# Performance work log

Measured on AMD Instinct MI355X. Metric: run time of the kernel, lower is better.

The kernel has to match this reference:

```python
import jax, jax.numpy as jnp
import numpy as np

F = 16       # num_field
D = 64       # embedding dim
N = 100000   # vocab size n
B = 2048     # batch
ORDER = 3
BETA = 1e-4
H = 64       # policy hidden (policy_layer=[64])


def build_levels(num_field, order):
    """Static reconstruction of create_mask recursion as integer index lists.
    At level t: V0 has r rows (row a = field a + t - 1); V_cur column k carries
    threshold thr[k]; the boolean mask is mask[a,k] = (a >= thr[k]); entries are
    enumerated row-major (matching torch boolean indexing). M_minus zeroes the
    last row (a == r-1) before the next level."""
    levels = []
    thr = np.arange(num_field - 1)  # create_mask(eye(F)) -> lower-tri incl diag
    r = num_field - 1
    for _ in range(2, order + 1):
        a_grid, k_grid = np.meshgrid(np.arange(r), np.arange(len(thr)), indexing='ij')
        sel = a_grid >= thr[None, :]
        rows = a_grid[sel]            # V0 row per selected interaction
        cols = k_grid[sel]            # V_cur column per selected interaction
        keep = np.nonzero(rows <= r - 2)[0]  # M_minus: drop last-row entries
        levels.append((rows, cols, keep))
        thr = rows[keep]
        r -= 1
    return levels

LEVELS = build_levels(F, ORDER)


def setup_inputs():
    key = jax.random.key(0)
    ks = jax.random.split(key, 9)
    x = jax.random.randint(ks[0], (B, F), 0, N)
    M = jax.random.normal(ks[1], (F, F), jnp.float32)
    w0 = jax.random.normal(ks[2], (1,), jnp.float32) * 0.01
    w_table = jax.random.normal(ks[3], (N,), jnp.float32) * 0.01
    V_table = jax.random.normal(ks[4], (N, D), jnp.float32) * 0.01
    Z_table = jax.random.normal(ks[5], (N, D), jnp.float32) * 0.01
    W1 = jax.random.normal(ks[6], (D, H), jnp.float32) * (1.0 / np.sqrt(D))
    b1 = jnp.zeros((H,), jnp.float32)
    W2 = jax.random.normal(ks[7], (H, 1), jnp.float32) * (1.0 / np.sqrt(H))
    b2 = jnp.zeros((1,), jnp.float32)
    return {"x": x, "M": M, "w0": w0, "w_table": w_table, "V_table": V_table,
            "Z_table": Z_table, "W1": W1, "b1": b1, "W2": W2, "b2": b2}


def reference(x, M, w0, w_table, V_table, Z_table, W1, b1, W2, b2):
    # forward_infer path (select=False)
    w = w_table[x]                                 # [B, F]
    V = V_table[x]                                 # [B, F, D]
    Z = jax.lax.stop_gradient(Z_table[x])          # .detach() in torch
    V0f = jnp.einsum('fg,bgd->bfd', M, V)          # M @ V
    Z0f = jnp.einsum('fg,bgd->bfd', M, Z)
    V_cur, V0 = V0f[:, :-1], V0f[:, 1:]
    Z_cur, Z0 = Z0f[:, :-1], Z0f[:, 1:]
    y = w0[0] + jnp.sum(w, axis=1)                 # [B]
    eps_key = jax.random.key(42)
    for li, (rows, cols, keep) in enumerate(LEVELS):
        # masked outer products, only at valid unique-combination slots
        V_sel = V0[:, rows] * V_cur[:, cols]       # [B, P, D]
        Z_sel = Z0[:, rows] * Z_cur[:, cols]       # [B, P, D]
        Wt = jnp.sum(V_sel, axis=-1)               # inference(): [B, P]
        h = jax.nn.relu(Z_sel @ W1 + b1)
        pro = jax.nn.sigmoid(h @ W2 + b2)[..., 0]  # [B, P]
        eps = jax.random.uniform(jax.random.fold_in(eps_key, li), pro.shape)
        S = (pro >= eps).astype(jnp.float32)       # Bernoulli selection
        y = y + jnp.sum(Wt * S, axis=-1)
        # slice for next order: V = V[:, M_minus]; V0 = V0[:, 1:]
        V_cur, Z_cur = V_sel[:, keep], Z_sel[:, keep]
        V0, Z0 = V0[:, 1:], Z0[:, 1:]
    regular = BETA * (jnp.sum(w * w) + jnp.sum(V_cur * V_cur))
    return y, regular
```

## Files before the change

kernel.cpp:

```cpp
#include <hip/hip_runtime.h>
#include <stdint.h>
#include <math.h>

#define NB    2048
#define NE    680
#define L1N   120
#define L2N   560
#define KEEP2 455
#define ROWP  68
#define NT    43
#define WLOS  72

#define THREEFRY_PARTITIONABLE 1

typedef __attribute__((ext_vector_type(8))) short bf16x8;
typedef __attribute__((ext_vector_type(4))) float f32x4;

union ABfrag { bf16x8 v; uint32_t u[4]; };

__device__ __forceinline__ uint32_t rotl32(uint32_t v, uint32_t d) {
  return (v << d) | (v >> (32u - d));
}

__device__ __forceinline__ uint32_t bf_rne(float f) {
  uint32_t u = __float_as_uint(f);
  return (u + 0x7fffu + ((u >> 16) & 1u)) >> 16;
}

__device__ __forceinline__ void tf2x32(uint32_t k0, uint32_t k1,
                                       uint32_t c0, uint32_t c1,
                                       uint32_t &o0, uint32_t &o1) {
  uint32_t ks2 = k0 ^ k1 ^ 0x1BD11BDAu;
  uint32_t x0 = c0 + k0;
  uint32_t x1 = c1 + k1;
#define TF_R(r) { x0 += x1; x1 = rotl32(x1, r); x1 ^= x0; }
  TF_R(13) TF_R(15) TF_R(26) TF_R(6)
  x0 += k1;  x1 += ks2 + 1u;
  TF_R(17) TF_R(29) TF_R(16) TF_R(24)
  x0 += ks2; x1 += k0 + 2u;
  TF_R(13) TF_R(15) TF_R(26) TF_R(6)
  x0 += k0;  x1 += k1 + 3u;
  TF_R(17) TF_R(29) TF_R(16) TF_R(24)
  x0 += k1;  x1 += ks2 + 4u;
  TF_R(13) TF_R(15) TF_R(26) TF_R(6)
  x0 += ks2; x1 += k0 + 5u;
#undef TF_R
  o0 = x0; o1 = x1;
}

__global__ __launch_bounds__(256, 8) void sfis_main(
    const int*   __restrict__ x,
    const float* __restrict__ M,
    const float* __restrict__ w0,
    const float* __restrict__ w_table,
    const float* __restrict__ V_table,
    const float* __restrict__ Z_table,
    const float* __restrict__ W1,
    const float* __restrict__ b1,
    const float* __restrict__ W2,
    const float* __restrict__ b2,
    float* __restrict__ out,
    float* __restrict__ reg_partial) {
  __shared__ __align__(16) float V0s[17 * ROWP];
  __shared__ __align__(16) float Z0s[17 * ROWP];
  __shared__ __align__(16) unsigned short W1loT[64 * WLOS];
  __shared__ unsigned short descs16[NT * 16];
  __shared__ float wts[NT * 16];
  __shared__ float t2s[NT * 16];
  __shared__ float W2s[64];
  __shared__ int xs[16];
  __shared__ float red8[8];
  __shared__ float wsum_s, w2sum_s;

  const int b   = blockIdx.x;
  const int tid = threadIdx.x;

  if (tid < 16) xs[tid] = x[b * 16 + tid];
  if (tid < 64) {
    W2s[tid] = W2[tid];
    V0s[16 * ROWP + tid] = 1.f;
    Z0s[16 * ROWP + tid] = 1.f;
  }
  for (int e = tid; e < NT * 16; e += 256) {
    int fi, fj, fl, lvl;
    if (e < L1N) {
      int a = 0;
      while ((a + 1) * (a + 2) / 2 <= e) ++a;
      int k = e - a * (a + 1) / 2;
      fi = a + 1; fj = k; fl = 16; lvl = 0;
    } else if (e < NE) {
      int e2 = e - L1N;
      int A = 0;
      while ((A + 1) * (A + 2) * (A + 3) / 6 <= e2) ++A;
      int k = e2 - A * (A + 1) * (A + 2) / 6;
      int a1 = 0;
      while ((a1 + 1) * (a1 + 2) / 2 <= k) ++a1;
      int k1 = k - a1 * (a1 + 1) / 2;
      fi = A + 2; fj = a1 + 1; fl = k1; lvl = 1;
    } else {
      fi = 16; fj = 16; fl = 16; lvl = 0;
    }
    descs16[e] = (unsigned short)((uint32_t)fi | ((uint32_t)fj << 5) |
                                  ((uint32_t)fl << 10) | ((uint32_t)lvl << 15));
  }
  for (int i = tid; i < 4096; i += 256) {
    int n = i & 63, k = i >> 6;
    float w = W1[i];
    uint32_t hb = bf_rne(w);
    float hf = __uint_as_float(hb << 16);
    W1loT[n * WLOS + k] = (unsigned short)bf_rne(w - hf);
  }
  __syncthreads();

  if (tid == 0) {
    float s = 0.f, s2 = 0.f;
    for (int f = 0; f < 16; ++f) {
      float wv = w_table[xs[f]];
      s += wv; s2 += wv * wv;
    }
    wsum_s = s; w2sum_s = s2;
  }
  for (int idx = tid; idx < 1024; idx += 256) {
    int f = idx >> 6, d = idx & 63;
    float av = 0.f, az = 0.f;
    for (int g = 0; g < 16; ++g) {
      float m = M[f * 16 + g];
      long off = (long)xs[g] * 64 + d;
      av = fmaf(m, V_table[off], av);
      az = fmaf(m, Z_table[off], az);
    }
    V0s[f * ROWP + d] = av;
    Z0s[f * ROWP + d] = az;
  }
  __syncthreads();

  float v2acc = 0.f;
  for (int e0 = 0; e0 < 768; e0 += 256) {
    const int e = e0 + tid;
    const bool valid = (e < NE);
    uint32_t dsc = valid ? (uint32_t)descs16[e] : 0x4210u;
    const int oI = (int)(dsc & 31) * ROWP;
    const int oJ = (int)((dsc >> 5) & 31) * ROWP;
    const int oL = (int)((dsc >> 10) & 31) * ROWP;
    const int lvl = (dsc >> 15) & 1;

    float wt = 0.f, vsq = 0.f;
    for (int dq = 0; dq < 16; ++dq) {
      float4 a = *(const float4*)&V0s[oJ + (dq << 2)];
      float4 c = *(const float4*)&V0s[oL + (dq << 2)];
      float4 v = *(const float4*)&V0s[oI + (dq << 2)];
      float p0 = v.x * (a.x * c.x);
      float p1 = v.y * (a.y * c.y);
      float p2 = v.z * (a.z * c.z);
      float p3 = v.w * (a.w * c.w);
      wt  += p0 + p1 + p2 + p3;
      vsq += p0 * p0 + p1 * p1 + p2 * p2 + p3 * p3;
    }
    if (valid) wts[e] = wt;
    if (valid && lvl && (uint32_t)(e - L1N) < (uint32_t)KEEP2) v2acc += vsq;
  }

  {
    const int lane = tid & 63;
    const int wave = tid >> 6;
    const int col  = lane & 15;
    const int kg   = lane >> 4;

    bf16x8 Bh[2][4];
#pragma unroll
    for (int ks = 0; ks < 2; ++ks)
#pragma unroll
      for (int c = 0; c < 4; ++c) {
        const float* wp = &W1[(ks * 32 + kg * 8) * 64 + c * 16 + col];
#pragma unroll
        for (int j = 0; j < 8; ++j)
          Bh[ks][c][j] = (short)bf_rne(wp[j * 64]);
      }
    float bv0 = b1[col], bv1 = b1[16 + col], bv2 = b1[32 + col], bv3 = b1[48 + col];

    for (int t = wave; t < NT; t += 4) {
      const int er = 16 * t + col;
      const uint32_t dsc = (uint32_t)descs16[er];
      const int oI = (int)(dsc & 31) * ROWP;
      const int oJ = (int)((dsc >> 5) & 31) * ROWP;
      const int oL = (int)((dsc >> 10) & 31) * ROWP;

      f32x4 acc[4];
      acc[0] = (f32x4){bv0, bv0, bv0, bv0};
      acc[1] = (f32x4){bv1, bv1, bv1, bv1};
      acc[2] = (f32x4){bv2, bv2, bv2, bv2};
      acc[3] = (f32x4){bv3, bv3, bv3, bv3};

#pragma unroll
      for (int ks = 0; ks < 2; ++ks) {
        const int kc = ks * 32 + kg * 8;
        float4 a0 = *(const float4*)&Z0s[oJ + kc];
        float4 c0 = *(const float4*)&Z0s[oL + kc];
        float4 z0 = *(const float4*)&Z0s[oI + kc];
        float4 a1 = *(const float4*)&Z0s[oJ + kc + 4];
        float4 c1 = *(const float4*)&Z0s[oL + kc + 4];
        float4 z1 = *(const float4*)&Z0s[oI + kc + 4];
        float z[8];
        z[0] = z0.x * (a0.x * c0.x);  z[1] = z0.y * (a0.y * c0.y);
        z[2] = z0.z * (a0.z * c0.z);  z[3] = z0.w * (a0.w * c0.w);
        z[4] = z1.x * (a1.x * c1.x);  z[5] = z1.y * (a1.y * c1.y);
        z[6] = z1.z * (a1.z * c1.z);  z[7] = z1.w * (a1.w * c1.w);

        ABfrag Ah, Al;
#pragma unroll
        for (int p = 0; p < 4; ++p) {
          uint32_t uz0 = __float_as_uint(z[2 * p]);
          uint32_t uz1 = __float_as_uint(z[2 * p + 1]);
          Ah.u[p] = __builtin_amdgcn_perm(uz1, uz0, 0x07060302u);
          float hf0 = __uint_as_float(uz0 & 0xffff0000u);
          float hf1 = __uint_as_float(uz1 & 0xffff0000u);
          uint32_t d0 = __float_as_uint(z[2 * p]     - hf0);
          uint32_t d1 = __float_as_uint(z[2 * p + 1] - hf1);
          d0 = d0 + 0x7fffu + ((d0 >> 16) & 1u);
          d1 = d1 + 0x7fffu + ((d1 >> 16) & 1u);
          Al.u[p] = __builtin_amdgcn_perm(d1, d0, 0x07060302u);
        }
#pragma unroll
        for (int c = 0; c < 4; ++c)
          acc[c] = __builtin_amdgcn_mfma_f32_16x16x32_bf16(Ah.v, Bh[ks][c], acc[c], 0, 0, 0);
#pragma unroll
        for (int c = 0; c < 4; ++c)
          acc[c] = __builtin_amdgcn_mfma_f32_16x16x32_bf16(Al.v, Bh[ks][c], acc[c], 0, 0, 0);
#pragma unroll
        for (int c = 0; c < 4; ++c) {
          bf16x8 Blf = *(const bf16x8*)&W1loT[(c * 16 + col) * WLOS + ks * 32 + kg * 8];
          acc[c] = __builtin_amdgcn_mfma_f32_16x16x32_bf16(Ah.v, Blf, acc[c], 0, 0, 0);
        }
      }

      float p0 = 0.f, p1 = 0.f, p2 = 0.f, p3 = 0.f;
#pragma unroll
      for (int c = 0; c < 4; ++c) {
        float w2v = W2s[c * 16 + col];
        p0 = fmaf(fmaxf(acc[c][0], 0.f), w2v, p0);
        p1 = fmaf(fmaxf(acc[c][1], 0.f), w2v, p1);
        p2 = fmaf(fmaxf(acc[c][2], 0.f), w2v, p2);
        p3 = fmaf(fmaxf(acc[c][3], 0.f), w2v, p3);
      }
#pragma unroll
      for (int m = 1; m < 16; m <<= 1) {
        p0 += __shfl_xor(p0, m, 16);
        p1 += __shfl_xor(p1, m, 16);
        p2 += __shfl_xor(p2, m, 16);
        p3 += __shfl_xor(p3, m, 16);
      }
      const int rb = 16 * t + kg * 4;
      if      (col == 0) t2s[rb + 0] = p0;
      else if (col == 1) t2s[rb + 1] = p1;
      else if (col == 2) t2s[rb + 2] = p2;
      else if (col == 3) t2s[rb + 3] = p3;
    }
  }
  __syncthreads();

  uint32_t fkA0, fkA1, fkB0, fkB1;
  tf2x32(0u, 42u, 0u, 0u, fkA0, fkA1);
  tf2x32(0u, 42u, 0u, 1u, fkB0, fkB1);
  const float b2v = b2[0];

  float yacc = 0.f;
  for (int e0 = 0; e0 < 768; e0 += 256) {
    const int e = e0 + tid;
    const bool valid = (e < NE);
    uint32_t dsc = valid ? (uint32_t)descs16[e] : 0x4210u;
    const int lvl = (dsc >> 15) & 1;

    float t2 = (valid ? t2s[e] : 0.f) + b2v;

    uint32_t Lsz  = lvl ? (uint32_t)L2N : (uint32_t)L1N;
    uint32_t lidx = lvl ? (uint32_t)(e - L1N) : (uint32_t)e;
    uint32_t kk0  = lvl ? fkB0 : fkA0;
    uint32_t kk1  = lvl ? fkB1 : fkA1;
    uint32_t gi   = (uint32_t)b * Lsz + lidx;
    uint32_t o0, o1, bits;
#if THREEFRY_PARTITIONABLE
    tf2x32(kk0, kk1, 0u, gi, o0, o1);
    bits = o0 ^ o1;
#else
    {
      uint32_t half = Lsz * (NB / 2);
      if (gi < half) { tf2x32(kk0, kk1, gi, gi + half, o0, o1); bits = o0; }
      else           { tf2x32(kk0, kk1, gi - half, gi, o0, o1); bits = o1; }
    }
#endif
    float eps = __uint_as_float((bits >> 9) | 0x3f800000u) - 1.0f;

    double ex = exp(-(double)t2);
    float pro = (float)(1.0 / (1.0 + ex));
    if (valid && pro >= eps) yacc += wts[e];
  }

  {
#pragma unroll
    for (int m = 32; m > 0; m >>= 1) {
      yacc  += __shfl_down(yacc, m, 64);
      v2acc += __shfl_down(v2acc, m, 64);
    }
    if ((tid & 63) == 0) {
      red8[tid >> 6]       = yacc;
      red8[4 + (tid >> 6)] = v2acc;
    }
    __syncthreads();
    if (tid == 0) {
      out[b] = w0[0] + wsum_s + ((red8[0] + red8[1]) + (red8[2] + red8[3]));
      reg_partial[b] = w2sum_s + ((red8[4] + red8[5]) + (red8[6] + red8[7]));
    }
  }
}

__global__ __launch_bounds__(256) void sfis_reduce(
    const float* __restrict__ reg_partial, float* __restrict__ out) {
  __shared__ float red[256];
  int tid = threadIdx.x;
  float s = 0.f;
  for (int i = tid; i < NB; i += 256) s += reg_partial[i];
  red[tid] = s;
  __syncthreads();
  for (int st = 128; st > 0; st >>= 1) {
    if (tid < st) red[tid] += red[tid + st];
    __syncthreads();
  }
  if (tid == 0) out[NB] = 1.0e-4f * red[0];
}

extern "C" void kernel_launch(void* const* d_in, const int* in_sizes, int n_in,
                              void* d_out, int out_size, void* d_ws, size_t ws_size,
                              hipStream_t stream) {
  (void)in_sizes; (void)n_in; (void)out_size; (void)ws_size;
  const int*   x       = (const int*)  d_in[0];
  const float* M       = (const float*)d_in[1];
  const float* w0      = (const float*)d_in[2];
  const float* w_table = (const float*)d_in[3];
  const float* V_table = (const float*)d_in[4];
  const float* Z_table = (const float*)d_in[5];
  const float* W1      = (const float*)d_in[6];
  const float* b1      = (const float*)d_in[7];
  const float* W2      = (const float*)d_in[8];
  const float* b2      = (const float*)d_in[9];
  float* out  = (float*)d_out;
  float* regp = (float*)d_ws;

  hipLaunchKernelGGL(sfis_main, dim3(NB), dim3(256), 0, stream,
                     x, M, w0, w_table, V_table, Z_table, W1, b1, W2, b2,
                     out, regp);
  hipLaunchKernelGGL(sfis_reduce, dim3(1), dim3(256), 0, stream, regp, out);
}
```

Before: 88.74 us.

## Precompute pair products in shared memory, widen blocks, keep W1 low part in registers

Computes the 105 second-order pair products of V and Z once per block into shared memory, so each third-order interaction needs one multiply instead of two, and the descriptor encoding changes to match. The block grows to 512 threads (8 waves) and the W1 low-bf16 split moves from a shared-memory table into per-lane registers. The sigmoid gate now uses fast float exp and falls back to double precision only when the result is close to the threshold. These trade extra shared memory and registers, plus an extra sync and product stage, for fewer LDS reads and cheaper transcendental work.

```diff
diff --git a/kernel.cpp b/kernel.cpp
--- a/kernel.cpp
+++ b/kernel.cpp
@@ -5,11 +5,10 @@
 #define NB    2048
 #define NE    680
 #define L1N   120
-#define L2N   560
 #define KEEP2 455
-#define ROWP  68
+#define PVS   68
 #define NT    43
-#define WLOS  72
+#define NSL   688
 
 #define THREEFRY_PARTITIONABLE 1
 
@@ -48,7 +47,7 @@
   o0 = x0; o1 = x1;
 }
 
-__global__ __launch_bounds__(256, 8) void sfis_main(
+__global__ __launch_bounds__(512, 4) void sfis_main(
     const int*   __restrict__ x,
     const float* __restrict__ M,
     const float* __restrict__ w0,
@@ -61,15 +60,14 @@
     const float* __restrict__ b2,
     float* __restrict__ out,
     float* __restrict__ reg_partial) {
-  __shared__ __align__(16) float V0s[17 * ROWP];
-  __shared__ __align__(16) float Z0s[17 * ROWP];
-  __shared__ __align__(16) unsigned short W1loT[64 * WLOS];
-  __shared__ unsigned short descs16[NT * 16];
-  __shared__ float wts[NT * 16];
-  __shared__ float t2s[NT * 16];
+  __shared__ __align__(16) float PV[123 * PVS];
+  __shared__ __align__(16) float PZ[123 * PVS];
+  __shared__ unsigned short descs16[NSL];
+  __shared__ float wts[NSL];
+  __shared__ float t2s[NSL];
   __shared__ float W2s[64];
   __shared__ int xs[16];
-  __shared__ float red8[8];
+  __shared__ float redY[8], redV[8];
   __shared__ float wsum_s, w2sum_s;
 
   const int b   = blockIdx.x;
@@ -78,37 +76,27 @@
   if (tid < 16) xs[tid] = x[b * 16 + tid];
   if (tid < 64) {
     W2s[tid] = W2[tid];
-    V0s[16 * ROWP + tid] = 1.f;
-    Z0s[16 * ROWP + tid] = 1.f;
-  }
-  for (int e = tid; e < NT * 16; e += 256) {
-    int fi, fj, fl, lvl;
+    PV[16 * PVS + tid] = 1.f;
+    PZ[16 * PVS + tid] = 1.f;
+  }
+  for (int e = tid; e < NSL; e += 512) {
+    int fi, prow, lvl;
     if (e < L1N) {
       int a = 0;
       while ((a + 1) * (a + 2) / 2 <= e) ++a;
       int k = e - a * (a + 1) / 2;
-      fi = a + 1; fj = k; fl = 16; lvl = 0;
+      fi = a + 1; prow = k; lvl = 0;
     } else if (e < NE) {
       int e2 = e - L1N;
       int A = 0;
       while ((A + 1) * (A + 2) * (A + 3) / 6 <= e2) ++A;
       int k = e2 - A * (A + 1) * (A + 2) / 6;
-      int a1 = 0;
-      while ((a1 + 1) * (a1 + 2) / 2 <= k) ++a1;
-      int k1 = k - a1 * (a1 + 1) / 2;
-      fi = A + 2; fj = a1 + 1; fl = k1; lvl = 1;
+      fi = A + 2; prow = 17 + k; lvl = 1;
     } else {
-      fi = 16; fj = 16; fl = 16; lvl = 0;
-    }
-    descs16[e] = (unsigned short)((uint32_t)fi | ((uint32_t)fj << 5) |
-                                  ((uint32_t)fl << 10) | ((uint32_t)lvl << 15));
-  }
-  for (int i = tid; i < 4096; i += 256) {
-    int n = i & 63, k = i >> 6;
-    float w = W1[i];
-    uint32_t hb = bf_rne(w);
-    float hf = __uint_as_float(hb << 16);
-    W1loT[n * WLOS + k] = (unsigned short)bf_rne(w - hf);
+      fi = 16; prow = 16; lvl = 0;
+    }
+    descs16[e] = (unsigned short)((uint32_t)fi | ((uint32_t)prow << 5) |
+                                  ((uint32_t)lvl << 12));
   }
   __syncthreads();
 
@@ -120,7 +108,7 @@
     }
     wsum_s = s; w2sum_s = s2;
   }
-  for (int idx = tid; idx < 1024; idx += 256) {
+  for (int idx = tid; idx < 1024; idx += 512) {
     int f = idx >> 6, d = idx & 63;
     float av = 0.f, az = 0.f;
     for (int g = 0; g < 16; ++g) {
@@ -129,35 +117,44 @@
       av = fmaf(m, V_table[off], av);
       az = fmaf(m, Z_table[off], az);
     }
-    V0s[f * ROWP + d] = av;
-    Z0s[f * ROWP + d] = az;
+    PV[f * PVS + d] = av;
+    PZ[f * PVS + d] = az;
+  }
+  __syncthreads();
+
+  for (int idx = tid; idx < 105 * 64; idx += 512) {
+    int m = idx >> 6, d = idx & 63;
+    int a1 = 0;
+    while ((a1 + 1) * (a1 + 2) / 2 <= m) ++a1;
+    int k1 = m - a1 * (a1 + 1) / 2;
+    PV[(17 + m) * PVS + d] = PV[(a1 + 1) * PVS + d] * PV[k1 * PVS + d];
+    PZ[(17 + m) * PVS + d] = PZ[(a1 + 1) * PVS + d] * PZ[k1 * PVS + d];
   }
   __syncthreads();
 
   float v2acc = 0.f;
-  for (int e0 = 0; e0 < 768; e0 += 256) {
+  for (int e0 = 0; e0 < 1024; e0 += 512) {
     const int e = e0 + tid;
-    const bool valid = (e < NE);
-    uint32_t dsc = valid ? (uint32_t)descs16[e] : 0x4210u;
-    const int oI = (int)(dsc & 31) * ROWP;
-    const int oJ = (int)((dsc >> 5) & 31) * ROWP;
-    const int oL = (int)((dsc >> 10) & 31) * ROWP;
-    const int lvl = (dsc >> 15) & 1;
-
-    float wt = 0.f, vsq = 0.f;
-    for (int dq = 0; dq < 16; ++dq) {
-      float4 a = *(const float4*)&V0s[oJ + (dq << 2)];
-      float4 c = *(const float4*)&V0s[oL + (dq << 2)];
-      float4 v = *(const float4*)&V0s[oI + (dq << 2)];
-      float p0 = v.x * (a.x * c.x);
-      float p1 = v.y * (a.y * c.y);
-      float p2 = v.z * (a.z * c.z);
-      float p3 = v.w * (a.w * c.w);
-      wt  += p0 + p1 + p2 + p3;
-      vsq += p0 * p0 + p1 * p1 + p2 * p2 + p3 * p3;
-    }
-    if (valid) wts[e] = wt;
-    if (valid && lvl && (uint32_t)(e - L1N) < (uint32_t)KEEP2) v2acc += vsq;
+    if (e < NE) {
+      uint32_t dsc = descs16[e];
+      const int oI = (int)(dsc & 31) * PVS;
+      const int oP = (int)((dsc >> 5) & 127) * PVS;
+      const int lvl = (dsc >> 12) & 1;
+
+      float wt = 0.f, vsq = 0.f;
+      for (int dq = 0; dq < 16; ++dq) {
+        float4 pv = *(const float4*)&PV[oP + (dq << 2)];
+        float4 vi = *(const float4*)&PV[oI + (dq << 2)];
+        float p0 = vi.x * pv.x;
+        float p1 = vi.y * pv.y;
+        float p2 = vi.z * pv.z;
+        float p3 = vi.w * pv.w;
+        wt  += p0 + p1 + p2 + p3;
+        vsq += p0 * p0 + p1 * p1 + p2 * p2 + p3 * p3;
+      }
+      wts[e] = wt;
+      if (lvl && (uint32_t)(e - L1N) < (uint32_t)KEEP2) v2acc += vsq;
+    }
   }
 
   {
@@ -166,24 +163,28 @@
     const int col  = lane & 15;
     const int kg   = lane >> 4;
 
-    bf16x8 Bh[2][4];
+    bf16x8 Bh[2][4], Bl[2][4];
 #pragma unroll
     for (int ks = 0; ks < 2; ++ks)
 #pragma unroll
       for (int c = 0; c < 4; ++c) {
         const float* wp = &W1[(ks * 32 + kg * 8) * 64 + c * 16 + col];
 #pragma unroll
-        for (int j = 0; j < 8; ++j)
-          Bh[ks][c][j] = (short)bf_rne(wp[j * 64]);
+        for (int j = 0; j < 8; ++j) {
+          float w = wp[j * 64];
+          uint32_t hb = bf_rne(w);
+          Bh[ks][c][j] = (short)hb;
+          float hf = __uint_as_float(hb << 16);
+          Bl[ks][c][j] = (short)bf_rne(w - hf);
+        }
       }
     float bv0 = b1[col], bv1 = b1[16 + col], bv2 = b1[32 + col], bv3 = b1[48 + col];
 
-    for (int t = wave; t < NT; t += 4) {
+    for (int t = wave; t < NT; t += 8) {
       const int er = 16 * t + col;
       const uint32_t dsc = (uint32_t)descs16[er];
-      const int oI = (int)(dsc & 31) * ROWP;
-      const int oJ = (int)((dsc >> 5) & 31) * ROWP;
-      const int oL = (int)((dsc >> 10) & 31) * ROWP;
+      const int oI = (int)(dsc & 31) * PVS;
+      const int oP = (int)((dsc >> 5) & 127) * PVS;
 
       f32x4 acc[4];
       acc[0] = (f32x4){bv0, bv0, bv0, bv0};
@@ -194,17 +195,15 @@
 #pragma unroll
       for (int ks = 0; ks < 2; ++ks) {
         const int kc = ks * 32 + kg * 8;
-        float4 a0 = *(const float4*)&Z0s[oJ + kc];
-        float4 c0 = *(const float4*)&Z0s[oL + kc];
-        float4 z0 = *(const float4*)&Z0s[oI + kc];
-        float4 a1 = *(const float4*)&Z0s[oJ + kc + 4];
-        float4 c1 = *(const float4*)&Z0s[oL + kc + 4];
-        float4 z1 = *(const float4*)&Z0s[oI + kc + 4];
+        float4 z0 = *(const float4*)&PZ[oI + kc];
+        float4 z1 = *(const float4*)&PZ[oI + kc + 4];
+        float4 q0 = *(const float4*)&PZ[oP + kc];
+        float4 q1 = *(const float4*)&PZ[oP + kc + 4];
         float z[8];
-        z[0] = z0.x * (a0.x * c0.x);  z[1] = z0.y * (a0.y * c0.y);
-        z[2] = z0.z * (a0.z * c0.z);  z[3] = z0.w * (a0.w * c0.w);
-        z[4] = z1.x * (a1.x * c1.x);  z[5] = z1.y * (a1.y * c1.y);
-        z[6] = z1.z * (a1.z * c1.z);  z[7] = z1.w * (a1.w * c1.w);
+        z[0] = z0.x * q0.x;  z[1] = z0.y * q0.y;
+        z[2] = z0.z * q0.z;  z[3] = z0.w * q0.w;
+        z[4] = z1.x * q1.x;  z[5] = z1.y * q1.y;
+        z[6] = z1.z * q1.z;  z[7] = z1.w * q1.w;
 
         ABfrag Ah, Al;
 #pragma unroll
@@ -227,10 +226,8 @@
         for (int c = 0; c < 4; ++c)
           acc[c] = __builtin_amdgcn_mfma_f32_16x16x32_bf16(Al.v, Bh[ks][c], acc[c], 0, 0, 0);
 #pragma unroll
-        for (int c = 0; c < 4; ++c) {
-          bf16x8 Blf = *(const bf16x8*)&W1loT[(c * 16 + col) * WLOS + ks * 32 + kg * 8];
-          acc[c] = __builtin_amdgcn_mfma_f32_16x16x32_bf16(Ah.v, Blf, acc[c], 0, 0, 0);
-        }
+        for (int c = 0; c < 4; ++c)
+          acc[c] = __builtin_amdgcn_mfma_f32_16x16x32_bf16(Ah.v, Bl[ks][c], acc[c], 0, 0, 0);
       }
 
       float p0 = 0.f, p1 = 0.f, p2 = 0.f, p3 = 0.f;
@@ -264,35 +261,42 @@
   const float b2v = b2[0];
 
   float yacc = 0.f;
-  for (int e0 = 0; e0 < 768; e0 += 256) {
+  for (int e0 = 0; e0 < 1024; e0 += 512) {
     const int e = e0 + tid;
-    const bool valid = (e < NE);
-    uint32_t dsc = valid ? (uint32_t)descs16[e] : 0x4210u;
-    const int lvl = (dsc >> 15) & 1;
-
-    float t2 = (valid ? t2s[e] : 0.f) + b2v;
-
-    uint32_t Lsz  = lvl ? (uint32_t)L2N : (uint32_t)L1N;
-    uint32_t lidx = lvl ? (uint32_t)(e - L1N) : (uint32_t)e;
-    uint32_t kk0  = lvl ? fkB0 : fkA0;
-    uint32_t kk1  = lvl ? fkB1 : fkA1;
-    uint32_t gi   = (uint32_t)b * Lsz + lidx;
-    uint32_t o0, o1, bits;
+    if (e < NE) {
+      uint32_t dsc = descs16[e];
+      const int lvl = (dsc >> 12) & 1;
+      float t2 = t2s[e] + b2v;
+
+      uint32_t Lsz  = lvl ? 560u : 120u;
+      uint32_t lidx = lvl ? (uint32_t)(e - L1N) : (uint32_t)e;
+      uint32_t kk0  = lvl ? fkB0 : fkA0;
+      uint32_t kk1  = lvl ? fkB1 : fkA1;
+      uint32_t gi   = (uint32_t)b * Lsz + lidx;
+      uint32_t o0, o1, bits;
 #if THREEFRY_PARTITIONABLE
-    tf2x32(kk0, kk1, 0u, gi, o0, o1);
-    bits = o0 ^ o1;
+      tf2x32(kk0, kk1, 0u, gi, o0, o1);
+      bits = o0 ^ o1;
 #else
-    {
-      uint32_t half = Lsz * (NB / 2);
-      if (gi < half) { tf2x32(kk0, kk1, gi, gi + half, o0, o1); bits = o0; }
-      else           { tf2x32(kk0, kk1, gi - half, gi, o0, o1); bits = o1; }
-    }
+      {
+        uint32_t half = Lsz * (NB / 2);
+        if (gi < half) { tf2x32(kk0, kk1, gi, gi + half, o0, o1); bits = o0; }
+        else           { tf2x32(kk0, kk1, gi - half, gi, o0, o1); bits = o1; }
+      }
 #endif
-    float eps = __uint_as_float((bits >> 9) | 0x3f800000u) - 1.0f;
-
-    double ex = exp(-(double)t2);
-    float pro = (float)(1.0 / (1.0 + ex));
-    if (valid && pro >= eps) yacc += wts[e];
+      float eps = __uint_as_float((bits >> 9) | 0x3f800000u) - 1.0f;
+
+      float pf = 1.0f / (1.0f + __expf(-t2));
+      bool gate;
+      if (fabsf(pf - eps) > 1e-4f) {
+        gate = (pf >= eps);
+      } else {
+        double ex = exp(-(double)t2);
+        float pro = (float)(1.0 / (1.0 + ex));
+        gate = (pro >= eps);
+      }
+      if (gate) yacc += wts[e];
+    }
   }
 
   {
@@ -302,13 +306,16 @@
       v2acc += __shfl_down(v2acc, m, 64);
     }
     if ((tid & 63) == 0) {
-      red8[tid >> 6]       = yacc;
-      red8[4 + (tid >> 6)] = v2acc;
+      redY[tid >> 6] = yacc;
+      redV[tid >> 6] = v2acc;
     }
     __syncthreads();
     if (tid == 0) {
-      out[b] = w0[0] + wsum_s + ((red8[0] + red8[1]) + (red8[2] + red8[3]));
-      reg_partial[b] = w2sum_s + ((red8[4] + red8[5]) + (red8[6] + red8[7]));
+      float ys = 0.f, vs = 0.f;
+#pragma unroll
+      for (int wv = 0; wv < 8; ++wv) { ys += redY[wv]; vs += redV[wv]; }
+      out[b] = w0[0] + wsum_s + ys;
+      reg_partial[b] = w2sum_s + vs;
     }
   }
 }
@@ -345,7 +352,7 @@
   float* out  = (float*)d_out;
   float* regp = (float*)d_ws;
 
-  hipLaunchKernelGGL(sfis_main, dim3(NB), dim3(256), 0, stream,
+  hipLaunchKernelGGL(sfis_main, dim3(NB), dim3(512), 0, stream,
                      x, M, w0, w_table, V_table, Z_table, W1, b1, W2, b2,
                      out, regp);
   hipLaunchKernelGGL(sfis_reduce, dim3(1), dim3(256), 0, stream, regp, out);
```

New measurement: 137.9 us. 1.55x slower.
